# Optimization experiments

Hardware: AMD Instinct MI355X
Metric: run time of the kernel (lower is better)

Reference implementation:

```python
import jax, jax.numpy as jnp
import numpy as np

SCALE = 16 / 8  # alpha / r

def setup_inputs() -> dict:
    key = jax.random.key(0)
    k1, k2, k3 = jax.random.split(key, 3)
    x = jax.random.normal(k1, (4, 2048, 4096), dtype=jnp.float32)
    A = jax.random.normal(k2, (4096, 8), dtype=jnp.float32)
    B = jax.random.normal(k3, (8, 4096), dtype=jnp.float32)
    return {"x": x, "A": A, "B": B}

def reference(x, A, B):
    # Faithful to torch module: materialize W = A @ B * scale, then x @ W
    W = (A @ B) * SCALE            # [dim, dim_out]
    return x @ W                   # [b, s, dim_out]
```

## Files before the change

kernel.cpp:

```cpp
#include <hip/hip_runtime.h>


#define DIM        4096
#define DIM4       1024
#define RANK       8
#define LORA_SCALE 2.0f
#define BLOCK      512
#define WAVES      8
#define ROWS       2
#define RPB        (WAVES * ROWS)
#define HALF_COLS  2048
#define HALF_Q     512

typedef float f32x4 __attribute__((ext_vector_type(4)));

__global__ __launch_bounds__(BLOCK, 2) void lora_fused_kernel(
    const float* __restrict__ x,
    const float* __restrict__ A,
    const float* __restrict__ B,
    float* __restrict__ out)
{
    __shared__ float sAt[RANK * HALF_COLS];
    __shared__ float tAll[RPB * RANK];

    const int tid  = threadIdx.x;
    const int wave = tid >> 6;
    const int lane = tid & 63;
    const size_t row0 = (size_t)blockIdx.x * RPB;

    const float4* __restrict__ A4 = (const float4*)A;
    const float4* __restrict__ B4 = (const float4*)B;
    const float4* __restrict__ x4 = (const float4*)x;
    const float4* sAt4 = (const float4*)sAt;

    float acc[ROWS][RANK];
#pragma unroll
    for (int m = 0; m < ROWS; ++m)
#pragma unroll
        for (int r = 0; r < RANK; ++r) acc[m][r] = 0.f;

    for (int h = 0; h < 2; ++h) {
        if (h) __syncthreads();
#pragma unroll
        for (int q = 0; q < 8; ++q) {
            const int idx = tid + q * BLOCK;
            const float4 v = A4[h * 4096 + idx];
            const int il = idx >> 1;
            const int rq = (idx & 1) * 4;
            sAt[(rq + 0) * HALF_COLS + il] = v.x;
            sAt[(rq + 1) * HALF_COLS + il] = v.y;
            sAt[(rq + 2) * HALF_COLS + il] = v.z;
            sAt[(rq + 3) * HALF_COLS + il] = v.w;
        }
        __syncthreads();

#pragma unroll
        for (int pb = 0; pb < 4; ++pb) {
            float4 xq[2][ROWS];
#pragma unroll
            for (int j = 0; j < 2; ++j)
#pragma unroll
                for (int m = 0; m < ROWS; ++m)
                    xq[j][m] = x4[(row0 + wave * ROWS + m) * DIM4
                                  + h * HALF_Q + (pb * 2 + j) * 64 + lane];
#pragma unroll
            for (int j = 0; j < 2; ++j) {
                const int il4 = (pb * 2 + j) * 64 + lane;
#pragma unroll
                for (int r = 0; r < RANK; ++r) {
                    const float4 a = sAt4[r * HALF_Q + il4];
#pragma unroll
                    for (int m = 0; m < ROWS; ++m)
                        acc[m][r] += xq[j][m].x * a.x + xq[j][m].y * a.y
                                   + xq[j][m].z * a.z + xq[j][m].w * a.w;
                }
            }
        }
    }

#pragma unroll
    for (int m = 0; m < ROWS; ++m) {
        float tval = 0.f;
#pragma unroll
        for (int r = 0; r < RANK; ++r) {
            float v = acc[m][r];
#pragma unroll
            for (int off = 1; off < 64; off <<= 1)
                v += __shfl_xor(v, off, 64);
            v *= LORA_SCALE;
            if (lane == r) tval = v;
        }
        if (lane < RANK)
            tAll[(wave * ROWS + m) * RANK + lane] = tval;
    }
    __syncthreads();

    const float4* tAll4 = (const float4*)tAll;
    f32x4* __restrict__ out4 = (f32x4*)out;
#pragma unroll
    for (int h3 = 0; h3 < 2; ++h3) {
        const int i4c = h3 * (WAVES * 64) + wave * 64 + lane;
        float4 b[RANK];
#pragma unroll
        for (int r = 0; r < RANK; ++r)
            b[r] = B4[r * DIM4 + i4c];
#pragma unroll 4
        for (int m = 0; m < RPB; ++m) {
            const float4 t0 = tAll4[m * 2 + 0];
            const float4 t1 = tAll4[m * 2 + 1];
            float4 o;
            o.x = t0.x * b[0].x; o.y = t0.x * b[0].y;
            o.z = t0.x * b[0].z; o.w = t0.x * b[0].w;
            o.x += t0.y * b[1].x; o.y += t0.y * b[1].y;
            o.z += t0.y * b[1].z; o.w += t0.y * b[1].w;
            o.x += t0.z * b[2].x; o.y += t0.z * b[2].y;
            o.z += t0.z * b[2].z; o.w += t0.z * b[2].w;
            o.x += t0.w * b[3].x; o.y += t0.w * b[3].y;
            o.z += t0.w * b[3].z; o.w += t0.w * b[3].w;
            o.x += t1.x * b[4].x; o.y += t1.x * b[4].y;
            o.z += t1.x * b[4].z; o.w += t1.x * b[4].w;
            o.x += t1.y * b[5].x; o.y += t1.y * b[5].y;
            o.z += t1.y * b[5].z; o.w += t1.y * b[5].w;
            o.x += t1.z * b[6].x; o.y += t1.z * b[6].y;
            o.z += t1.z * b[6].z; o.w += t1.z * b[6].w;
            o.x += t1.w * b[7].x; o.y += t1.w * b[7].y;
            o.z += t1.w * b[7].z; o.w += t1.w * b[7].w;
            f32x4 ov;
            ov.x = o.x; ov.y = o.y; ov.z = o.z; ov.w = o.w;
            __builtin_nontemporal_store(ov, &out4[(row0 + m) * DIM4 + i4c]);
        }
    }
}

extern "C" void kernel_launch(void* const* d_in, const int* in_sizes, int n_in,
                              void* d_out, int out_size, void* d_ws, size_t ws_size,
                              hipStream_t stream) {
    const float* x = (const float*)d_in[0];
    const float* A = (const float*)d_in[1];
    const float* B = (const float*)d_in[2];
    float* out = (float*)d_out;

    const int rows = in_sizes[0] / DIM;
    lora_fused_kernel<<<rows / RPB, BLOCK, 0, stream>>>(x, A, B, out);
}
```

Before: 257.2 us.

## Split fused LoRA kernel into separate x@A and y@B kernels via workspace

Splits the single fused kernel into two launches. The first computes the rank-8 projection y = x@A*scale and writes it to the workspace. The second expands y@B over a 2D grid of row and column tiles with a swizzled block order, smaller blocks and higher occupancy. The aim is to decouple the read-bound phase from the write-bound phase so each can use its own launch shape. The cost is an extra kernel launch and a small round trip of y through global memory. The x-loading loop is also regrouped to issue four column chunks per iteration.

```diff
diff --git a/kernel.cpp b/kernel.cpp
--- a/kernel.cpp
+++ b/kernel.cpp
@@ -5,37 +5,35 @@
 #define DIM4       1024
 #define RANK       8
 #define LORA_SCALE 2.0f
-#define BLOCK      512
-#define WAVES      8
-#define ROWS       2
-#define RPB        (WAVES * ROWS)
+
+typedef float f32x4 __attribute__((ext_vector_type(4)));
+
+#define YBLOCK     512
+#define YWAVES     8
+#define YROWS      2
+#define YRPB       (YWAVES * YROWS)
 #define HALF_COLS  2048
 #define HALF_Q     512
 
-typedef float f32x4 __attribute__((ext_vector_type(4)));
-
-__global__ __launch_bounds__(BLOCK, 2) void lora_fused_kernel(
+__global__ __launch_bounds__(YBLOCK, 2) void lora_xa_kernel(
     const float* __restrict__ x,
     const float* __restrict__ A,
-    const float* __restrict__ B,
-    float* __restrict__ out)
+    float* __restrict__ y)
 {
     __shared__ float sAt[RANK * HALF_COLS];
-    __shared__ float tAll[RPB * RANK];
 
     const int tid  = threadIdx.x;
     const int wave = tid >> 6;
     const int lane = tid & 63;
-    const size_t row0 = (size_t)blockIdx.x * RPB;
+    const size_t row0 = (size_t)blockIdx.x * YRPB;
 
     const float4* __restrict__ A4 = (const float4*)A;
-    const float4* __restrict__ B4 = (const float4*)B;
     const float4* __restrict__ x4 = (const float4*)x;
     const float4* sAt4 = (const float4*)sAt;
 
-    float acc[ROWS][RANK];
+    float acc[YROWS][RANK];
 #pragma unroll
-    for (int m = 0; m < ROWS; ++m)
+    for (int m = 0; m < YROWS; ++m)
 #pragma unroll
         for (int r = 0; r < RANK; ++r) acc[m][r] = 0.f;
 
@@ -43,7 +41,7 @@
         if (h) __syncthreads();
 #pragma unroll
         for (int q = 0; q < 8; ++q) {
-            const int idx = tid + q * BLOCK;
+            const int idx = tid + q * YBLOCK;
             const float4 v = A4[h * 4096 + idx];
             const int il = idx >> 1;
             const int rq = (idx & 1) * 4;
@@ -55,31 +53,31 @@
         __syncthreads();
 
 #pragma unroll
-        for (int pb = 0; pb < 4; ++pb) {
-            float4 xq[2][ROWS];
+        for (int pb = 0; pb < 2; ++pb) {
+            float4 xq[4][YROWS];
 #pragma unroll
-            for (int j = 0; j < 2; ++j)
+            for (int p = 0; p < 4; ++p)
 #pragma unroll
-                for (int m = 0; m < ROWS; ++m)
-                    xq[j][m] = x4[(row0 + wave * ROWS + m) * DIM4
-                                  + h * HALF_Q + (pb * 2 + j) * 64 + lane];
+                for (int m = 0; m < YROWS; ++m)
+                    xq[p][m] = x4[(row0 + wave * YROWS + m) * DIM4
+                                  + h * HALF_Q + (pb * 4 + p) * 64 + lane];
 #pragma unroll
-            for (int j = 0; j < 2; ++j) {
-                const int il4 = (pb * 2 + j) * 64 + lane;
+            for (int p = 0; p < 4; ++p) {
+                const int il4 = (pb * 4 + p) * 64 + lane;
 #pragma unroll
                 for (int r = 0; r < RANK; ++r) {
                     const float4 a = sAt4[r * HALF_Q + il4];
 #pragma unroll
-                    for (int m = 0; m < ROWS; ++m)
-                        acc[m][r] += xq[j][m].x * a.x + xq[j][m].y * a.y
-                                   + xq[j][m].z * a.z + xq[j][m].w * a.w;
+                    for (int m = 0; m < YROWS; ++m)
+                        acc[m][r] += xq[p][m].x * a.x + xq[p][m].y * a.y
+                                   + xq[p][m].z * a.z + xq[p][m].w * a.w;
                 }
             }
         }
     }
 
 #pragma unroll
-    for (int m = 0; m < ROWS; ++m) {
+    for (int m = 0; m < YROWS; ++m) {
         float tval = 0.f;
 #pragma unroll
         for (int r = 0; r < RANK; ++r) {
@@ -91,44 +89,63 @@
             if (lane == r) tval = v;
         }
         if (lane < RANK)
-            tAll[(wave * ROWS + m) * RANK + lane] = tval;
+            y[(row0 + wave * YROWS + m) * RANK + lane] = tval;
     }
-    __syncthreads();
+}
 
-    const float4* tAll4 = (const float4*)tAll;
+#define OBLOCK     256
+#define OWAVES     4
+#define OROWS      16
+#define OCOLQ      256
+
+__global__ __launch_bounds__(OBLOCK, 6) void lora_yb_kernel(
+    const float* __restrict__ y,
+    const float* __restrict__ B,
+    float* __restrict__ out)
+{
+    const int swz    = (blockIdx.x & 7) * 256 + (blockIdx.x >> 3);
+    const int colblk = swz >> 9;
+    const int rowblk = swz & 511;
+
+    const int tid  = threadIdx.x;
+    const int wave = tid >> 6;
+    const int lane = tid & 63;
+    const size_t row0 = (size_t)rowblk * OROWS;
+    const int i4c = colblk * OCOLQ + wave * 64 + lane;
+
+    const float4* __restrict__ B4 = (const float4*)B;
+    const float4* __restrict__ y4 = (const float4*)y;
     f32x4* __restrict__ out4 = (f32x4*)out;
+
+    float4 b[RANK];
 #pragma unroll
-    for (int h3 = 0; h3 < 2; ++h3) {
-        const int i4c = h3 * (WAVES * 64) + wave * 64 + lane;
-        float4 b[RANK];
-#pragma unroll
-        for (int r = 0; r < RANK; ++r)
-            b[r] = B4[r * DIM4 + i4c];
+    for (int r = 0; r < RANK; ++r)
+        b[r] = B4[r * DIM4 + i4c];
+
 #pragma unroll 4
-        for (int m = 0; m < RPB; ++m) {
-            const float4 t0 = tAll4[m * 2 + 0];
-            const float4 t1 = tAll4[m * 2 + 1];
-            float4 o;
-            o.x = t0.x * b[0].x; o.y = t0.x * b[0].y;
-            o.z = t0.x * b[0].z; o.w = t0.x * b[0].w;
-            o.x += t0.y * b[1].x; o.y += t0.y * b[1].y;
-            o.z += t0.y * b[1].z; o.w += t0.y * b[1].w;
-            o.x += t0.z * b[2].x; o.y += t0.z * b[2].y;
-            o.z += t0.z * b[2].z; o.w += t0.z * b[2].w;
-            o.x += t0.w * b[3].x; o.y += t0.w * b[3].y;
-            o.z += t0.w * b[3].z; o.w += t0.w * b[3].w;
-            o.x += t1.x * b[4].x; o.y += t1.x * b[4].y;
-            o.z += t1.x * b[4].z; o.w += t1.x * b[4].w;
-            o.x += t1.y * b[5].x; o.y += t1.y * b[5].y;
-            o.z += t1.y * b[5].z; o.w += t1.y * b[5].w;
-            o.x += t1.z * b[6].x; o.y += t1.z * b[6].y;
-            o.z += t1.z * b[6].z; o.w += t1.z * b[6].w;
-            o.x += t1.w * b[7].x; o.y += t1.w * b[7].y;
-            o.z += t1.w * b[7].z; o.w += t1.w * b[7].w;
-            f32x4 ov;
-            ov.x = o.x; ov.y = o.y; ov.z = o.z; ov.w = o.w;
-            __builtin_nontemporal_store(ov, &out4[(row0 + m) * DIM4 + i4c]);
-        }
+    for (int m = 0; m < OROWS; ++m) {
+        const float4 t0 = y4[(row0 + m) * 2 + 0];
+        const float4 t1 = y4[(row0 + m) * 2 + 1];
+        float4 o;
+        o.x = t0.x * b[0].x; o.y = t0.x * b[0].y;
+        o.z = t0.x * b[0].z; o.w = t0.x * b[0].w;
+        o.x += t0.y * b[1].x; o.y += t0.y * b[1].y;
+        o.z += t0.y * b[1].z; o.w += t0.y * b[1].w;
+        o.x += t0.z * b[2].x; o.y += t0.z * b[2].y;
+        o.z += t0.z * b[2].z; o.w += t0.z * b[2].w;
+        o.x += t0.w * b[3].x; o.y += t0.w * b[3].y;
+        o.z += t0.w * b[3].z; o.w += t0.w * b[3].w;
+        o.x += t1.x * b[4].x; o.y += t1.x * b[4].y;
+        o.z += t1.x * b[4].z; o.w += t1.x * b[4].w;
+        o.x += t1.y * b[5].x; o.y += t1.y * b[5].y;
+        o.z += t1.y * b[5].z; o.w += t1.y * b[5].w;
+        o.x += t1.z * b[6].x; o.y += t1.z * b[6].y;
+        o.z += t1.z * b[6].z; o.w += t1.z * b[6].w;
+        o.x += t1.w * b[7].x; o.y += t1.w * b[7].y;
+        o.z += t1.w * b[7].z; o.w += t1.w * b[7].w;
+        f32x4 ov;
+        ov.x = o.x; ov.y = o.y; ov.z = o.z; ov.w = o.w;
+        __builtin_nontemporal_store(ov, &out4[(row0 + m) * DIM4 + i4c]);
     }
 }
 
@@ -139,7 +156,10 @@
     const float* A = (const float*)d_in[1];
     const float* B = (const float*)d_in[2];
     float* out = (float*)d_out;
+    float* y   = (float*)d_ws;
 
     const int rows = in_sizes[0] / DIM;
-    lora_fused_kernel<<<rows / RPB, BLOCK, 0, stream>>>(x, A, B, out);
+
+    lora_xa_kernel<<<rows / YRPB, YBLOCK, 0, stream>>>(x, A, y);
+    lora_yb_kernel<<<(rows / OROWS) * (DIM4 / OCOLQ), OBLOCK, 0, stream>>>(y, B, out);
 }
```

Result: faster. 244.0 us (-5.2%).
